# Performance work log

Measured on AMD Instinct MI355X. Metric: run time of the kernel, lower is better.

Reference implementation:

```python
import jax, jax.numpy as jnp
import numpy as np

NUM_SITES = 64
BOND_DIM = 64
PHYS_DIM = 2
BATCH = 8192
INIT_STD = 0.125  # 1/sqrt(bond_dim)
EPS_AMP = 1e-12
EPS_LOG = 1e-30


def setup_inputs() -> dict:
    key = jax.random.key(0)
    k_cfg, k_l, k_b, k_r = jax.random.split(key, 4)
    configurations = jax.random.randint(k_cfg, (BATCH, NUM_SITES), 0, PHYS_DIM, dtype=jnp.int32)
    left = jax.random.normal(k_l, (PHYS_DIM, BOND_DIM), dtype=jnp.float32) * INIT_STD
    bulk = jax.random.normal(k_b, (NUM_SITES - 2, BOND_DIM, PHYS_DIM, BOND_DIM), dtype=jnp.float32) * INIT_STD
    right = jax.random.normal(k_r, (BOND_DIM, PHYS_DIM), dtype=jnp.float32) * INIT_STD
    return {"configurations": configurations, "left": left, "bulk": bulk, "right": right}


def _psi(configurations, left, bulk, right):
    # configurations: [B, S] int; left: [d, D]; bulk: [S-2, D, d, D]; right: [D, d]
    B = configurations.shape[0]
    env0 = left[configurations[:, 0]]  # [B, D]
    cfg_mid = configurations[:, 1:-1].T  # [S-2, B]

    def step(env, xs):
        site_t, idx = xs  # site_t: [D, d, D], idx: [B]
        D = site_t.shape[0]
        # env @ site (contract left bond), then gather the per-sample physical slice
        tmp = (env @ site_t.reshape(D, -1)).reshape(B, PHYS_DIM, D)  # [B, d, D]
        env = jnp.take_along_axis(tmp, idx[:, None, None], axis=1)[:, 0, :]  # [B, D]
        return env, None

    env, _ = jax.lax.scan(step, env0, (bulk, cfg_mid))
    cols = jnp.take(right, configurations[:, -1], axis=1).T  # [B, D]
    return jnp.sum(env * cols, axis=1)  # [B]


def _log_norm(left, bulk, right):
    env0 = left.T @ left  # [D, D]  (real dtype -> conj trivial)

    def step(carry, site_t):
        env, log_scale = carry
        sm = jnp.transpose(site_t, (1, 0, 2))  # [d, D, D]
        env = jnp.einsum('pdi,de,pej->ij', sm, env, sm)  # sum_p A_p^H env A_p
        scale = jnp.maximum(jnp.max(jnp.abs(env)), EPS_LOG)
        return (env / scale, log_scale + jnp.log(scale)), None

    (env, log_scale), _ = jax.lax.scan(step, (env0, jnp.zeros((), left.dtype)), bulk)
    z = jnp.sum(right * (env @ right))
    return jnp.log(jnp.maximum(z, EPS_LOG)) + log_scale


def reference(configurations, left, bulk, right):
    psi = _psi(configurations, left, bulk, right)
    abs_sq = jnp.maximum(psi * psi, EPS_AMP)
    log_z = _log_norm(left, bulk, right)
    nll = -(jnp.log(abs_sq) - log_z)
    return jnp.mean(nll)
```

## Files before the change

kernel.cpp:

```cpp
#include <hip/hip_runtime.h>
#include <math.h>

#define NBULK 62
#define SB    72

typedef __attribute__((ext_vector_type(8))) short bf8_t;
typedef __attribute__((ext_vector_type(4))) float f4_t;

#define MFMA(a, b, c) __builtin_amdgcn_mfma_f32_16x16x32_bf16((a), (b), (c), 0, 0, 0)

__device__ __forceinline__ unsigned short f2bf(float f) {
    unsigned int u = __float_as_uint(f);
    return (unsigned short)((u + 0x7FFFu + ((u >> 16) & 1u)) >> 16);
}
__device__ __forceinline__ float bf2f(unsigned short h) {
    return __uint_as_float(((unsigned int)h) << 16);
}

__device__ __forceinline__ void gload16(const void* g, void* l) {
    __builtin_amdgcn_global_load_lds(
        (const __attribute__((address_space(1))) unsigned int*)g,
        (__attribute__((address_space(3))) unsigned int*)l, 16, 0, 0);
}

#define WS_E_OFF   1024
#define WS_B_OFF   6144
#define WS_BT_OFF  45056
#define WS_MR_OFF  1060864


extern "C" __global__ __launch_bounds__(256)
void mps_precompute(const float* __restrict__ bulkG,
                    unsigned short* __restrict__ BTg,
                    unsigned short* __restrict__ MRg)
{
    __shared__ unsigned short BTl[8192];
    __shared__ unsigned short MRl[8192];
    const int s = blockIdx.x, tid = threadIdx.x;
    const float4* src = (const float4*)(bulkG + (size_t)s * 8192);
    for (int c = 0; c < 8; ++c) {
        int idx = tid + c * 256;
        float4 v = src[idx];
        int f  = idx * 4;
        int kk = f >> 7;
        int p  = (f >> 6) & 1;
        int j  = f & 63;
        unsigned short b0 = f2bf(v.x), b1 = f2bf(v.y), b2 = f2bf(v.z), b3 = f2bf(v.w);
        int n = p * 64 + kk;
        int off = n * 64 + (((j >> 3) ^ (n & 7)) << 3) + (j & 7);
        MRl[off + 0] = b0; MRl[off + 1] = b1; MRl[off + 2] = b2; MRl[off + 3] = b3;
        unsigned short bb[4] = {b0, b1, b2, b3};
        #pragma unroll
        for (int t2 = 0; t2 < 4; ++t2) {
            int n2 = p * 64 + j + t2;
            BTl[n2 * 64 + (((kk >> 3) ^ (n2 & 7)) << 3) + (kk & 7)] = bb[t2];
        }
    }
    __syncthreads();
    const uint4* bt4 = (const uint4*)BTl;
    const uint4* mr4 = (const uint4*)MRl;
    uint4* btg = (uint4*)(BTg + (size_t)s * 8192);
    uint4* mrg = (uint4*)(MRg + (size_t)s * 8192);
    for (int c = 0; c < 4; ++c) {
        int idx = tid + c * 256;
        btg[idx] = bt4[idx];
        mrg[idx] = mr4[idx];
    }
}

extern "C" __global__ __launch_bounds__(256)
void mps_main(const int* __restrict__ cfgG, const float* __restrict__ leftG,
              const float* __restrict__ rightG, float* __restrict__ wsF,
              const unsigned short* __restrict__ BTg,
              const unsigned short* __restrict__ MRg)
{
    extern __shared__ char smem[];
    unsigned short* smem16 = (unsigned short*)smem;
    const int tid  = threadIdx.x;
    const int bid  = blockIdx.x;
    const int wv   = tid >> 6;
    const int lane = tid & 63;
    const int quad = lane >> 4;
    const int ln   = lane & 15;

    if (bid >= 2) {
        unsigned short* Bb0  = smem16;
        unsigned short* Bb1  = Bb0 + 8192;
        unsigned short* env  = Bb1 + 8192;
        unsigned char*  selT = (unsigned char*)(env + 64 * SB);

        const int s0 = (bid - 2) * 64;
        {
            int m = tid >> 2, part = tid & 3;
            const int* row = cfgG + (size_t)(s0 + m) * 64 + part * 16;
            #pragma unroll
            for (int q = 0; q < 4; ++q) {
                int4 v = *(const int4*)(row + q * 4);
                int cb = part * 16 + q * 4;
                selT[(cb + 0) * 64 + m] = (unsigned char)v.x;
                selT[(cb + 1) * 64 + m] = (unsigned char)v.y;
                selT[(cb + 2) * 64 + m] = (unsigned char)v.z;
                selT[(cb + 3) * 64 + m] = (unsigned char)v.w;
            }
        }
        {
            const char* g0 = (const char*)BTg;
            for (int c = 0; c < 4; ++c) {
                int chunk = wv * 4 + c;
                gload16(g0 + chunk * 1024 + (size_t)lane * 16, (char*)Bb0 + chunk * 1024);
            }
        }
        __syncthreads();

        bf8_t Af[2];
        {
            int sel0 = selT[0 * 64 + wv * 16 + ln];
            const float* lp0 = leftG + sel0 * 64;
            #pragma unroll
            for (int h = 0; h < 2; ++h) {
                float4 a = *(const float4*)(lp0 + h * 32 + quad * 8);
                float4 b = *(const float4*)(lp0 + h * 32 + quad * 8 + 4);
                bf8_t t;
                t[0] = (short)f2bf(a.x); t[1] = (short)f2bf(a.y);
                t[2] = (short)f2bf(a.z); t[3] = (short)f2bf(a.w);
                t[4] = (short)f2bf(b.x); t[5] = (short)f2bf(b.y);
                t[6] = (short)f2bf(b.z); t[7] = (short)f2bf(b.w);
                Af[h] = t;
            }
        }

        for (int t = 0; t < NBULK; ++t) {
            __syncthreads();
            unsigned short* B = (t & 1) ? Bb1 : Bb0;
            if (t + 1 < NBULK) {
                const char* gn = (const char*)(BTg + (size_t)(t + 1) * 8192);
                char* l = (char*)((t & 1) ? Bb0 : Bb1);
                for (int c = 0; c < 4; ++c) {
                    int chunk = wv * 4 + c;
                    gload16(gn + chunk * 1024 + (size_t)lane * 16, l + chunk * 1024);
                }
            }
            bf8_t Bf[2][4][2];
            #pragma unroll
            for (int b2 = 0; b2 < 2; ++b2)
                #pragma unroll
                for (int ct = 0; ct < 4; ++ct) {
                    int row = b2 * 64 + ct * 16 + ln;
                    #pragma unroll
                    for (int h = 0; h < 2; ++h)
                        Bf[b2][ct][h] = *(const bf8_t*)(B + row * 64 + (((h * 4 + quad) ^ (ln & 7)) << 3));
                }
            f4_t acc[2][4];
            #pragma unroll
            for (int b2 = 0; b2 < 2; ++b2)
                #pragma unroll
                for (int ct = 0; ct < 4; ++ct) {
                    f4_t a = {0.f, 0.f, 0.f, 0.f};
                    a = MFMA(Af[0], Bf[b2][ct][0], a);
                    a = MFMA(Af[1], Bf[b2][ct][1], a);
                    acc[b2][ct] = a;
                }
            unsigned int sv = *(const unsigned int*)(selT + (t + 1) * 64 + wv * 16 + quad * 4);
            #pragma unroll
            for (int ct = 0; ct < 4; ++ct)
                #pragma unroll
                for (int r = 0; r < 4; ++r) {
                    float v = ((sv >> (8 * r)) & 1u) ? acc[1][ct][r] : acc[0][ct][r];
                    env[(wv * 16 + quad * 4 + r) * SB + ct * 16 + ln] = f2bf(v);
                }
            Af[0] = *(const bf8_t*)(env + (wv * 16 + ln) * SB + quad * 8);
            Af[1] = *(const bf8_t*)(env + (wv * 16 + ln) * SB + 32 + quad * 8);
        }
        {
            int selL = selT[63 * 64 + wv * 16 + ln];
            bf8_t e0 = *(const bf8_t*)(env + (wv * 16 + ln) * SB + quad * 16);
            bf8_t e1 = *(const bf8_t*)(env + (wv * 16 + ln) * SB + quad * 16 + 8);
            float p = 0.f;
            #pragma unroll
            for (int j = 0; j < 8; ++j)
                p = fmaf(bf2f((unsigned short)e0[j]), rightG[(quad * 16 + j) * 2 + selL], p);
            #pragma unroll
            for (int j = 0; j < 8; ++j)
                p = fmaf(bf2f((unsigned short)e1[j]), rightG[(quad * 16 + 8 + j) * 2 + selL], p);
            p += __shfl_xor(p, 16);
            p += __shfl_xor(p, 32);
            float lp = logf(fmaxf(p * p, 1e-12f));
            lp += __shfl_xor(lp, 1); lp += __shfl_xor(lp, 2);
            lp += __shfl_xor(lp, 4); lp += __shfl_xor(lp, 8);
            if (lane == 0) atomicAdd(&wsF[0], lp);
        }
    } else {
        unsigned short* Ebf = smem16;
        unsigned short* St0 = Ebf + 64 * SB;
        unsigned short* St1 = St0 + 64 * SB;
        unsigned short* Ms0 = St1 + 64 * SB;
        unsigned short* Ms1 = Ms0 + 8192;
        float* wred = (float*)(Ms1 + 8192);

        const bool fwd = (bid == 0);
        const unsigned short* srcbase = fwd ? BTg : MRg;
        {
            int i = tid >> 2, jq = tid & 3;
            for (int jj = 0; jj < 16; ++jj) {
                int j = jq * 16 + jj;
                float v;
                if (fwd) v = leftG[i] * leftG[j] + leftG[64 + i] * leftG[64 + j];
                else     v = rightG[i * 2] * rightG[j * 2] + rightG[i * 2 + 1] * rightG[j * 2 + 1];
                Ebf[i * SB + j] = f2bf(v);
            }
        }
        {
            int st = fwd ? 0 : 61;
            const char* g = (const char*)(srcbase + (size_t)st * 8192);
            for (int c = 0; c < 4; ++c) {
                int chunk = wv * 4 + c;
                gload16(g + chunk * 1024 + (size_t)lane * 16, (char*)Ms0 + chunk * 1024);
            }
        }
        float lsum = 0.f;
        const int p   = wv >> 1;
        const int ntb = (wv & 1) * 2;
        const int mta = (wv >> 1) * 2;
        const int nta = (wv & 1) * 2;
        unsigned short* Stp = p ? St1 : St0;

        for (int k = 0; k < 31; ++k) {
            __syncthreads();
            unsigned short* M = (k & 1) ? Ms1 : Ms0;
            if (k + 1 < 31) {
                int sn = fwd ? (k + 1) : (61 - (k + 1));
                const char* g = (const char*)(srcbase + (size_t)sn * 8192);
                char* l = (char*)((k & 1) ? Ms0 : Ms1);
                for (int c = 0; c < 4; ++c) {
                    int chunk = wv * 4 + c;
                    gload16(g + chunk * 1024 + (size_t)lane * 16, l + chunk * 1024);
                }
            }
            float inv = 1.f;
            if (k > 0) {
                const float* wp = wred + ((k - 1) & 1) * 4;
                float mm = fmaxf(fmaxf(wp[0], wp[1]), fmaxf(wp[2], wp[3]));
                float sc = fmaxf(mm, 1e-30f);
                inv = 1.f / sc;
                if (tid == 0) lsum += logf(sc);
            }
            {
                bf8_t Af2[4][2];
                #pragma unroll
                for (int mt = 0; mt < 4; ++mt)
                    #pragma unroll
                    for (int h = 0; h < 2; ++h)
                        Af2[mt][h] = *(const bf8_t*)(Ebf + (mt * 16 + ln) * SB + h * 32 + quad * 8);
                #pragma unroll
                for (int c = 0; c < 2; ++c) {
                    int nt = ntb + c;
                    int row = p * 64 + nt * 16 + ln;
                    bf8_t B0 = *(const bf8_t*)(M + row * 64 + (((0 + quad) ^ (ln & 7)) << 3));
                    bf8_t B1 = *(const bf8_t*)(M + row * 64 + (((4 + quad) ^ (ln & 7)) << 3));
                    #pragma unroll
                    for (int mt = 0; mt < 4; ++mt) {
                        f4_t a = {0.f, 0.f, 0.f, 0.f};
                        a = MFMA(Af2[mt][0], B0, a);
                        a = MFMA(Af2[mt][1], B1, a);
                        ushort4 pk;
                        pk.x = f2bf(a[0]); pk.y = f2bf(a[1]); pk.z = f2bf(a[2]); pk.w = f2bf(a[3]);
                        *(ushort4*)(Stp + (nt * 16 + ln) * SB + mt * 16 + quad * 4) = pk;
                    }
                }
            }
            __syncthreads();
            {
                bf8_t Aw[2][2][2], Bw[2][2][2];
                #pragma unroll
                for (int pp = 0; pp < 2; ++pp)
                    #pragma unroll
                    for (int mi = 0; mi < 2; ++mi)
                        #pragma unroll
                        for (int h = 0; h < 2; ++h)
                            Aw[pp][mi][h] = *(const bf8_t*)(M + (pp * 64 + (mta + mi) * 16 + ln) * 64
                                                              + (((h * 4 + quad) ^ (ln & 7)) << 3));
                #pragma unroll
                for (int pp = 0; pp < 2; ++pp)
                    #pragma unroll
                    for (int ni = 0; ni < 2; ++ni)
                        #pragma unroll
                        for (int h = 0; h < 2; ++h)
                            Bw[pp][ni][h] = *(const bf8_t*)((pp ? St1 : St0)
                                                            + ((nta + ni) * 16 + ln) * SB + h * 32 + quad * 8);
                float mx = 0.f;
                #pragma unroll
                for (int mi = 0; mi < 2; ++mi)
                    #pragma unroll
                    for (int ni = 0; ni < 2; ++ni) {
                        f4_t a = {0.f, 0.f, 0.f, 0.f};
                        #pragma unroll
                        for (int pp = 0; pp < 2; ++pp)
                            #pragma unroll
                            for (int h = 0; h < 2; ++h)
                                a = MFMA(Aw[pp][mi][h], Bw[pp][ni][h], a);
                        #pragma unroll
                        for (int r = 0; r < 4; ++r) {
                            float val = a[r] * inv;
                            mx = fmaxf(mx, fabsf(val));
                            Ebf[((mta + mi) * 16 + quad * 4 + r) * SB + (nta + ni) * 16 + ln] = f2bf(val);
                        }
                    }
                #pragma unroll
                for (int off = 32; off > 0; off >>= 1)
                    mx = fmaxf(mx, __shfl_xor(mx, off));
                if (lane == 0) wred[(k & 1) * 4 + wv] = mx;
            }
        }
        __syncthreads();
        float* dst = wsF + (fwd ? WS_E_OFF : WS_B_OFF);
        for (int c = 0; c < 16; ++c) {
            int idx = tid + c * 256;
            dst[idx] = bf2f(Ebf[(idx >> 6) * SB + (idx & 63)]);
        }
        if (tid == 0) wsF[fwd ? 1 : 2] = lsum;
    }
}

extern "C" __global__ void mps_finalize(const float* __restrict__ wsF, float* __restrict__ out)
{
    const int lane = threadIdx.x;
    const float* E  = wsF + WS_E_OFF;
    const float* Bm = wsF + WS_B_OFF;
    float a = 0.f;
    #pragma unroll 8
    for (int j = 0; j < 64; ++j)
        a = fmaf(E[lane * 64 + j], Bm[lane * 64 + j], a);
    #pragma unroll
    for (int off = 32; off > 0; off >>= 1)
        a += __shfl_down(a, off);
    if (lane == 0) {
        const float z = fmaxf(a, 1e-30f);
        const float log_z = logf(z) + wsF[1] + wsF[2];
        out[0] = log_z - wsF[0] * (1.0f / 8192.0f);
    }
}

extern "C" void kernel_launch(void* const* d_in, const int* in_sizes, int n_in,
                              void* d_out, int out_size, void* d_ws, size_t ws_size,
                              hipStream_t stream)
{
    const int*   cfg   = (const int*)d_in[0];
    const float* left  = (const float*)d_in[1];
    const float* bulk  = (const float*)d_in[2];
    const float* right = (const float*)d_in[3];
    float* wsF = (float*)d_ws;
    unsigned short* BTg = (unsigned short*)((char*)d_ws + WS_BT_OFF);
    unsigned short* MRg = (unsigned short*)((char*)d_ws + WS_MR_OFF);

    hipMemsetAsync(d_ws, 0, 16, stream);
    mps_precompute<<<dim3(62), dim3(256), 0, stream>>>(bulk, BTg, MRg);
    mps_main<<<dim3(130), dim3(256), 60480, stream>>>(cfg, left, right, wsF, BTg, MRg);
    mps_finalize<<<dim3(1), dim3(64), 0, stream>>>(wsF, (float*)d_out);
}
```

Baseline: 119.4 us.

## Load site matrices straight into registers and fold finalize into main kernel

Drops the LDS double-buffered global_load_lds staging of per-site bf16 matrices. Each wave now reads its MFMA fragments from global memory (L2) directly into registers, with a two-deep register prefetch of the next site. It also removes the memset and the separate finalize launch: precompute zeroes the accumulators and the last block to finish, found through an atomic counter, does the final reduction. This cuts LDS use and two launches but raises register pressure and puts the scattered 16-byte global loads on the serial dependency chain.

```diff
diff --git a/kernel.cpp b/kernel.cpp
--- a/kernel.cpp
+++ b/kernel.cpp
@@ -3,6 +3,8 @@
 
 #define NBULK 62
 #define SB    72
+#define NPSI  128
+#define NBLK  130
 
 typedef __attribute__((ext_vector_type(8))) short bf8_t;
 typedef __attribute__((ext_vector_type(4))) float f4_t;
@@ -15,12 +17,6 @@
 }
 __device__ __forceinline__ float bf2f(unsigned short h) {
     return __uint_as_float(((unsigned int)h) << 16);
-}
-
-__device__ __forceinline__ void gload16(const void* g, void* l) {
-    __builtin_amdgcn_global_load_lds(
-        (const __attribute__((address_space(1))) unsigned int*)g,
-        (__attribute__((address_space(3))) unsigned int*)l, 16, 0, 0);
 }
 
 #define WS_E_OFF   1024
@@ -32,11 +28,16 @@
 extern "C" __global__ __launch_bounds__(256)
 void mps_precompute(const float* __restrict__ bulkG,
                     unsigned short* __restrict__ BTg,
-                    unsigned short* __restrict__ MRg)
+                    unsigned short* __restrict__ MRg,
+                    float* __restrict__ wsF)
 {
     __shared__ unsigned short BTl[8192];
     __shared__ unsigned short MRl[8192];
     const int s = blockIdx.x, tid = threadIdx.x;
+    if (s == 0 && tid == 0) {
+        wsF[0] = 0.f; wsF[1] = 0.f; wsF[2] = 0.f;
+        ((int*)wsF)[3] = 0;
+    }
     const float4* src = (const float4*)(bulkG + (size_t)s * 8192);
     for (int c = 0; c < 8; ++c) {
         int idx = tid + c * 256;
@@ -68,11 +69,12 @@
     }
 }
 
-extern "C" __global__ __launch_bounds__(256)
+extern "C" __global__ __launch_bounds__(256, 1)
 void mps_main(const int* __restrict__ cfgG, const float* __restrict__ leftG,
               const float* __restrict__ rightG, float* __restrict__ wsF,
               const unsigned short* __restrict__ BTg,
-              const unsigned short* __restrict__ MRg)
+              const unsigned short* __restrict__ MRg,
+              float* __restrict__ outG)
 {
     extern __shared__ char smem[];
     unsigned short* smem16 = (unsigned short*)smem;
@@ -84,9 +86,7 @@
     const int ln   = lane & 15;
 
     if (bid >= 2) {
-        unsigned short* Bb0  = smem16;
-        unsigned short* Bb1  = Bb0 + 8192;
-        unsigned short* env  = Bb1 + 8192;
+        unsigned short* env  = smem16;
         unsigned char*  selT = (unsigned char*)(env + 64 * SB);
 
         const int s0 = (bid - 2) * 64;
@@ -103,61 +103,51 @@
                 selT[(cb + 3) * 64 + m] = (unsigned char)v.w;
             }
         }
-        {
-            const char* g0 = (const char*)BTg;
-            for (int c = 0; c < 4; ++c) {
-                int chunk = wv * 4 + c;
-                gload16(g0 + chunk * 1024 + (size_t)lane * 16, (char*)Bb0 + chunk * 1024);
-            }
-        }
         __syncthreads();
 
-        bf8_t Af[2];
+        int boff[2][4][2];
+        #pragma unroll
+        for (int b2 = 0; b2 < 2; ++b2)
+            #pragma unroll
+            for (int ct = 0; ct < 4; ++ct) {
+                int row = b2 * 64 + ct * 16 + ln;
+                #pragma unroll
+                for (int h = 0; h < 2; ++h)
+                    boff[b2][ct][h] = row * 64 + (((h * 4 + quad) ^ (ln & 7)) << 3);
+            }
+
+        bf8_t Af0, Af1;
         {
             int sel0 = selT[0 * 64 + wv * 16 + ln];
             const float* lp0 = leftG + sel0 * 64;
-            #pragma unroll
-            for (int h = 0; h < 2; ++h) {
-                float4 a = *(const float4*)(lp0 + h * 32 + quad * 8);
-                float4 b = *(const float4*)(lp0 + h * 32 + quad * 8 + 4);
-                bf8_t t;
-                t[0] = (short)f2bf(a.x); t[1] = (short)f2bf(a.y);
-                t[2] = (short)f2bf(a.z); t[3] = (short)f2bf(a.w);
-                t[4] = (short)f2bf(b.x); t[5] = (short)f2bf(b.y);
-                t[6] = (short)f2bf(b.z); t[7] = (short)f2bf(b.w);
-                Af[h] = t;
-            }
-        }
-
-        for (int t = 0; t < NBULK; ++t) {
-            __syncthreads();
-            unsigned short* B = (t & 1) ? Bb1 : Bb0;
-            if (t + 1 < NBULK) {
-                const char* gn = (const char*)(BTg + (size_t)(t + 1) * 8192);
-                char* l = (char*)((t & 1) ? Bb0 : Bb1);
-                for (int c = 0; c < 4; ++c) {
-                    int chunk = wv * 4 + c;
-                    gload16(gn + chunk * 1024 + (size_t)lane * 16, l + chunk * 1024);
-                }
-            }
-            bf8_t Bf[2][4][2];
+            bf8_t t0, t1;
+            #pragma unroll
+            for (int j = 0; j < 8; ++j) {
+                t0[j] = (short)f2bf(lp0[quad * 8 + j]);
+                t1[j] = (short)f2bf(lp0[32 + quad * 8 + j]);
+            }
+            Af0 = t0; Af1 = t1;
+        }
+
+        auto loadB = [&](bf8_t (&B)[2][4][2], int t) {
+            const unsigned short* base = BTg + (size_t)t * 8192;
             #pragma unroll
             for (int b2 = 0; b2 < 2; ++b2)
                 #pragma unroll
-                for (int ct = 0; ct < 4; ++ct) {
-                    int row = b2 * 64 + ct * 16 + ln;
+                for (int ct = 0; ct < 4; ++ct)
                     #pragma unroll
                     for (int h = 0; h < 2; ++h)
-                        Bf[b2][ct][h] = *(const bf8_t*)(B + row * 64 + (((h * 4 + quad) ^ (ln & 7)) << 3));
-                }
+                        B[b2][ct][h] = *(const bf8_t*)(base + boff[b2][ct][h]);
+        };
+        auto psite = [&](bf8_t (&B)[2][4][2], int t) {
             f4_t acc[2][4];
             #pragma unroll
             for (int b2 = 0; b2 < 2; ++b2)
                 #pragma unroll
                 for (int ct = 0; ct < 4; ++ct) {
                     f4_t a = {0.f, 0.f, 0.f, 0.f};
-                    a = MFMA(Af[0], Bf[b2][ct][0], a);
-                    a = MFMA(Af[1], Bf[b2][ct][1], a);
+                    a = MFMA(Af0, B[b2][ct][0], a);
+                    a = MFMA(Af1, B[b2][ct][1], a);
                     acc[b2][ct] = a;
                 }
             unsigned int sv = *(const unsigned int*)(selT + (t + 1) * 64 + wv * 16 + quad * 4);
@@ -168,8 +158,17 @@
                     float v = ((sv >> (8 * r)) & 1u) ? acc[1][ct][r] : acc[0][ct][r];
                     env[(wv * 16 + quad * 4 + r) * SB + ct * 16 + ln] = f2bf(v);
                 }
-            Af[0] = *(const bf8_t*)(env + (wv * 16 + ln) * SB + quad * 8);
-            Af[1] = *(const bf8_t*)(env + (wv * 16 + ln) * SB + 32 + quad * 8);
+            Af0 = *(const bf8_t*)(env + (wv * 16 + ln) * SB + quad * 8);
+            Af1 = *(const bf8_t*)(env + (wv * 16 + ln) * SB + 32 + quad * 8);
+        };
+
+        bf8_t BfA[2][4][2], BfB[2][4][2];
+        loadB(BfA, 0);
+        for (int tt = 0; tt < 31; ++tt) {
+            loadB(BfB, 2 * tt + 1);
+            psite(BfA, 2 * tt);
+            if (tt < 30) loadB(BfA, 2 * tt + 2);
+            psite(BfB, 2 * tt + 1);
         }
         {
             int selL = selT[63 * 64 + wv * 16 + ln];
@@ -193,9 +192,7 @@
         unsigned short* Ebf = smem16;
         unsigned short* St0 = Ebf + 64 * SB;
         unsigned short* St1 = St0 + 64 * SB;
-        unsigned short* Ms0 = St1 + 64 * SB;
-        unsigned short* Ms1 = Ms0 + 8192;
-        float* wred = (float*)(Ms1 + 8192);
+        float* wred = (float*)(St1 + 64 * SB);
 
         const bool fwd = (bid == 0);
         const unsigned short* srcbase = fwd ? BTg : MRg;
@@ -209,14 +206,6 @@
                 Ebf[i * SB + j] = f2bf(v);
             }
         }
-        {
-            int st = fwd ? 0 : 61;
-            const char* g = (const char*)(srcbase + (size_t)st * 8192);
-            for (int c = 0; c < 4; ++c) {
-                int chunk = wv * 4 + c;
-                gload16(g + chunk * 1024 + (size_t)lane * 16, (char*)Ms0 + chunk * 1024);
-            }
-        }
         float lsum = 0.f;
         const int p   = wv >> 1;
         const int ntb = (wv & 1) * 2;
@@ -224,18 +213,42 @@
         const int nta = (wv & 1) * 2;
         unsigned short* Stp = p ? St1 : St0;
 
-        for (int k = 0; k < 31; ++k) {
+        int o1[2][2], o2[2][2][2];
+        #pragma unroll
+        for (int c = 0; c < 2; ++c) {
+            int row = p * 64 + (ntb + c) * 16 + ln;
+            #pragma unroll
+            for (int h = 0; h < 2; ++h)
+                o1[c][h] = row * 64 + (((h * 4 + quad) ^ (ln & 7)) << 3);
+        }
+        #pragma unroll
+        for (int pp = 0; pp < 2; ++pp)
+            #pragma unroll
+            for (int mi = 0; mi < 2; ++mi) {
+                int row = pp * 64 + (mta + mi) * 16 + ln;
+                #pragma unroll
+                for (int h = 0; h < 2; ++h)
+                    o2[pp][mi][h] = row * 64 + (((h * 4 + quad) ^ (ln & 7)) << 3);
+            }
+
+        auto loadM = [&](bf8_t (&M1)[2][2], bf8_t (&M2)[2][2][2], int site) {
+            const unsigned short* base = srcbase + (size_t)site * 8192;
+            #pragma unroll
+            for (int c = 0; c < 2; ++c)
+                #pragma unroll
+                for (int h = 0; h < 2; ++h)
+                    M1[c][h] = *(const bf8_t*)(base + o1[c][h]);
+            #pragma unroll
+            for (int pp = 0; pp < 2; ++pp)
+                #pragma unroll
+                for (int mi = 0; mi < 2; ++mi)
+                    #pragma unroll
+                    for (int h = 0; h < 2; ++h)
+                        M2[pp][mi][h] = *(const bf8_t*)(base + o2[pp][mi][h]);
+        };
+        auto nsite = [&](bf8_t (&M1)[2][2], bf8_t (&M2)[2][2][2],
+                         bf8_t (&N1)[2][2], bf8_t (&N2)[2][2][2], int k, bool pf) {
             __syncthreads();
-            unsigned short* M = (k & 1) ? Ms1 : Ms0;
-            if (k + 1 < 31) {
-                int sn = fwd ? (k + 1) : (61 - (k + 1));
-                const char* g = (const char*)(srcbase + (size_t)sn * 8192);
-                char* l = (char*)((k & 1) ? Ms0 : Ms1);
-                for (int c = 0; c < 4; ++c) {
-                    int chunk = wv * 4 + c;
-                    gload16(g + chunk * 1024 + (size_t)lane * 16, l + chunk * 1024);
-                }
-            }
             float inv = 1.f;
             if (k > 0) {
                 const float* wp = wred + ((k - 1) & 1) * 4;
@@ -244,6 +257,7 @@
                 inv = 1.f / sc;
                 if (tid == 0) lsum += logf(sc);
             }
+            if (pf) loadM(N1, N2, fwd ? (k + 1) : (61 - (k + 1)));
             {
                 bf8_t Af2[4][2];
                 #pragma unroll
@@ -254,14 +268,11 @@
                 #pragma unroll
                 for (int c = 0; c < 2; ++c) {
                     int nt = ntb + c;
-                    int row = p * 64 + nt * 16 + ln;
-                    bf8_t B0 = *(const bf8_t*)(M + row * 64 + (((0 + quad) ^ (ln & 7)) << 3));
-                    bf8_t B1 = *(const bf8_t*)(M + row * 64 + (((4 + quad) ^ (ln & 7)) << 3));
                     #pragma unroll
                     for (int mt = 0; mt < 4; ++mt) {
                         f4_t a = {0.f, 0.f, 0.f, 0.f};
-                        a = MFMA(Af2[mt][0], B0, a);
-                        a = MFMA(Af2[mt][1], B1, a);
+                        a = MFMA(Af2[mt][0], M1[c][0], a);
+                        a = MFMA(Af2[mt][1], M1[c][1], a);
                         ushort4 pk;
                         pk.x = f2bf(a[0]); pk.y = f2bf(a[1]); pk.z = f2bf(a[2]); pk.w = f2bf(a[3]);
                         *(ushort4*)(Stp + (nt * 16 + ln) * SB + mt * 16 + quad * 4) = pk;
@@ -270,15 +281,7 @@
             }
             __syncthreads();
             {
-                bf8_t Aw[2][2][2], Bw[2][2][2];
-                #pragma unroll
-                for (int pp = 0; pp < 2; ++pp)
-                    #pragma unroll
-                    for (int mi = 0; mi < 2; ++mi)
-                        #pragma unroll
-                        for (int h = 0; h < 2; ++h)
-                            Aw[pp][mi][h] = *(const bf8_t*)(M + (pp * 64 + (mta + mi) * 16 + ln) * 64
-                                                              + (((h * 4 + quad) ^ (ln & 7)) << 3));
+                bf8_t Bw[2][2][2];
                 #pragma unroll
                 for (int pp = 0; pp < 2; ++pp)
                     #pragma unroll
@@ -286,7 +289,7 @@
                         #pragma unroll
                         for (int h = 0; h < 2; ++h)
                             Bw[pp][ni][h] = *(const bf8_t*)((pp ? St1 : St0)
-                                                            + ((nta + ni) * 16 + ln) * SB + h * 32 + quad * 8);
+                                            + ((nta + ni) * 16 + ln) * SB + h * 32 + quad * 8);
                 float mx = 0.f;
                 #pragma unroll
                 for (int mi = 0; mi < 2; ++mi)
@@ -297,7 +300,7 @@
                         for (int pp = 0; pp < 2; ++pp)
                             #pragma unroll
                             for (int h = 0; h < 2; ++h)
-                                a = MFMA(Aw[pp][mi][h], Bw[pp][ni][h], a);
+                                a = MFMA(M2[pp][mi][h], Bw[pp][ni][h], a);
                         #pragma unroll
                         for (int r = 0; r < 4; ++r) {
                             float val = a[r] * inv;
@@ -310,7 +313,16 @@
                     mx = fmaxf(mx, __shfl_xor(mx, off));
                 if (lane == 0) wred[(k & 1) * 4 + wv] = mx;
             }
-        }
+        };
+
+        bf8_t M1A[2][2], M2A[2][2][2], M1B[2][2], M2B[2][2][2];
+        loadM(M1A, M2A, fwd ? 0 : 61);
+        for (int kk = 0; kk < 15; ++kk) {
+            nsite(M1A, M2A, M1B, M2B, 2 * kk,     true);
+            nsite(M1B, M2B, M1A, M2A, 2 * kk + 1, true);
+        }
+        nsite(M1A, M2A, M1B, M2B, 30, false);
+
         __syncthreads();
         float* dst = wsF + (fwd ? WS_E_OFF : WS_B_OFF);
         for (int c = 0; c < 16; ++c) {
@@ -319,24 +331,38 @@
         }
         if (tid == 0) wsF[fwd ? 1 : 2] = lsum;
     }
-}
-
-extern "C" __global__ void mps_finalize(const float* __restrict__ wsF, float* __restrict__ out)
-{
-    const int lane = threadIdx.x;
-    const float* E  = wsF + WS_E_OFF;
-    const float* Bm = wsF + WS_B_OFF;
-    float a = 0.f;
-    #pragma unroll 8
-    for (int j = 0; j < 64; ++j)
-        a = fmaf(E[lane * 64 + j], Bm[lane * 64 + j], a);
-    #pragma unroll
-    for (int off = 32; off > 0; off >>= 1)
-        a += __shfl_down(a, off);
-    if (lane == 0) {
-        const float z = fmaxf(a, 1e-30f);
-        const float log_z = logf(z) + wsF[1] + wsF[2];
-        out[0] = log_z - wsF[0] * (1.0f / 8192.0f);
+
+    __syncthreads();
+    __threadfence();
+    __syncthreads();
+    int* eflag = (int*)smem;
+    if (tid == 0) {
+        int old = atomicAdd((int*)wsF + 3, 1);
+        eflag[0] = (old == NBLK - 1) ? 1 : 0;
+    }
+    __syncthreads();
+    if (eflag[0]) {
+        __threadfence();
+        const float4* E  = (const float4*)(wsF + WS_E_OFF);
+        const float4* Bm = (const float4*)(wsF + WS_B_OFF);
+        float a = 0.f;
+        #pragma unroll
+        for (int c = 0; c < 4; ++c) {
+            int idx = tid + c * 256;
+            float4 e = E[idx], b = Bm[idx];
+            a += e.x * b.x + e.y * b.y + e.z * b.z + e.w * b.w;
+        }
+        #pragma unroll
+        for (int off = 32; off > 0; off >>= 1)
+            a += __shfl_down(a, off);
+        float* ered = (float*)smem + 8;
+        if ((tid & 63) == 0) ered[tid >> 6] = a;
+        __syncthreads();
+        if (tid == 0) {
+            float z = fmaxf(ered[0] + ered[1] + ered[2] + ered[3], 1e-30f);
+            float log_z = logf(z) + wsF[1] + wsF[2];
+            outG[0] = log_z - wsF[0] * (1.0f / 8192.0f);
+        }
     }
 }
 
@@ -352,8 +378,6 @@
     unsigned short* BTg = (unsigned short*)((char*)d_ws + WS_BT_OFF);
     unsigned short* MRg = (unsigned short*)((char*)d_ws + WS_MR_OFF);
 
-    hipMemsetAsync(d_ws, 0, 16, stream);
-    mps_precompute<<<dim3(62), dim3(256), 0, stream>>>(bulk, BTg, MRg);
-    mps_main<<<dim3(130), dim3(256), 60480, stream>>>(cfg, left, right, wsF, BTg, MRg);
-    mps_finalize<<<dim3(1), dim3(64), 0, stream>>>(wsF, (float*)d_out);
-}
+    mps_precompute<<<dim3(62), dim3(256), 0, stream>>>(bulk, BTg, MRg, wsF);
+    mps_main<<<dim3(NBLK), dim3(256), 28672, stream>>>(cfg, left, right, wsF, BTg, MRg, (float*)d_out);
+}
```

Result: slower. 123.0 us (+3.1%).
